# Kernel tuning notes

Hardware: AMD Instinct MI355X
Metric: run time of the kernel (lower is better)

## Reference

```python
import jax, jax.numpy as jnp
import numpy as np

N_NODES = 100_000
N_EDGES = 1_000_000
H = 128
NUM_STATES = 4
UPPER_T, LOWER_T, NUM_ITERS, TEMP_EVAL = 1.0, 0.1, 10000, 0.1


def temp_by_step(step, upper, lower, num_iters, temp_eval):
    # Python-level schedule: eval temp at step == -1, else linear anneal.
    if step == -1:
        return temp_eval
    frac = min(step / num_iters, 1.0)
    return upper + (lower - upper) * frac


def from_binary_states(states):
    # [*, k] bits -> integer id in [0, 2**k)
    weights = 2 ** jnp.arange(states.shape[-1])
    return (states * weights).sum(-1)


def setup_inputs() -> dict:
    key = jax.random.key(0)
    ks = jax.random.split(key, 20)
    N, E, h = N_NODES, N_EDGES, H
    node_states = jax.random.randint(ks[0], (N, NUM_STATES), 0, 2)
    edge_states = jax.random.randint(ks[1], (E, NUM_STATES), 0, 2)
    scalars = jax.random.normal(ks[2], (E, 1), jnp.float32)
    # first N edges are self-loops ordered by node id (required by the module's
    # node_scalars = scalars[src == dst] indexing convention)
    loops = jnp.arange(N)
    src = jax.random.randint(ks[3], (E - N,), 0, N)
    dst = jax.random.randint(ks[4], (E - N,), 0, N)
    dst = jnp.where(dst == src, (dst + 1) % N, dst)  # no accidental self-loops
    edge_index = jnp.stack([jnp.concatenate([loops, src]),
                            jnp.concatenate([loops, dst])])
    batched_reverse_idx = jax.random.randint(ks[5], (E,), 0, E)
    batch_scalars = jax.random.normal(ks[6], (E, 1, 1), jnp.float32)
    s = 0.02
    params = dict(
        node_emb=s * jax.random.normal(ks[7], (2 ** NUM_STATES, h), jnp.float32),
        edge_emb=s * jax.random.normal(ks[8], (2 ** NUM_STATES, h), jnp.float32),
        combine_W=s * jax.random.normal(ks[9], (2 * h, h), jnp.float32),
        combine_b=jnp.zeros((h,), jnp.float32),
        keep_W=s * jax.random.normal(ks[10], (h, 2), jnp.float32),
        keep_b=jnp.zeros((2,), jnp.float32),
        push_W=s * jax.random.normal(ks[11], (h, 2), jnp.float32),
        push_b=jnp.zeros((2,), jnp.float32),
        push_node_W=s * jax.random.normal(ks[12], (h, 2), jnp.float32),
        push_node_b=jnp.zeros((2,), jnp.float32),
        increment_W=s * jax.random.normal(ks[13], (h, 2), jnp.float32),
        increment_b=jnp.zeros((2,), jnp.float32),
    )
    return dict(node_states=node_states, edge_states=edge_states, scalars=scalars,
                edge_index=edge_index, batched_reverse_idx=batched_reverse_idx,
                batch_scalars=batch_scalars, processor_step=0, training_step=0,
                **params)


def reference(node_states, edge_states, scalars, edge_index, batched_reverse_idx,
              batch_scalars, processor_step, training_step,
              node_emb, edge_emb, combine_W, combine_b, keep_W, keep_b,
              push_W, push_b, push_node_W, push_node_b,
              increment_W, increment_b):
    N = node_states.shape[0]
    tau = temp_by_step(int(training_step), UPPER_T, LOWER_T, NUM_ITERS, TEMP_EVAL)
    # use_noise = config.use_noise (False) and training_step != -1 -> False

    node_fts = node_emb[from_binary_states(node_states)]   # [N, h]
    edge_fts = edge_emb[from_binary_states(edge_states)]   # [E, h]
    src, dst = edge_index[0], edge_index[1]
    fts = jnp.concatenate([edge_fts[batched_reverse_idx], node_fts[src]], axis=1)
    fts = fts @ combine_W + combine_b                       # [E, h]

    s = scalars.reshape(-1)                                 # [E]

    def pair_gumbel_first(W, b):
        # grouped (per-edge pair) softmax; take first component (== [::2])
        logits = (fts @ W + b) / tau                        # [E, 2]
        return jax.nn.softmax(logits, axis=-1)[:, 0]

    increment = 1.0 * pair_gumbel_first(increment_W, increment_b)
    keep = s * pair_gumbel_first(keep_W, keep_b)

    # push: first N edges are self-loops, self-loop of node i is edge i
    push_wo = pair_gumbel_first(push_W, push_b)
    push_w = pair_gumbel_first(push_node_W, push_node_b)
    node_scalars = s[:N]                                    # scalars at self-loops
    s_wo = s - node_scalars[dst]
    s_w = s_wo + node_scalars[src]
    acc = (jax.ops.segment_sum(push_wo * s_wo, dst, num_segments=N)
           + jax.ops.segment_sum(push_w * s_w, dst, num_segments=N))  # [N]
    edge_push = jnp.zeros_like(s).at[:N].set(acc)           # nonzero only on self-loops

    new_scalars = (increment + keep + edge_push)[:, None]   # [E, 1]
    target = batch_scalars[:, processor_step]               # [E, 1]
    loss = jnp.mean((target - new_scalars) ** 2)
    return new_scalars, loss
```

## Files before the change

kernel.cpp:

```cpp
#include <hip/hip_runtime.h>
#include <math.h>

#define N_NODES 100000
#define N_EDGES 1000000
#define HDIM 128
#define N_NONLOOP (N_EDGES - N_NODES)

typedef float  vfloat4 __attribute__((ext_vector_type(4)));

__device__ __forceinline__ float get_invtau(const int* __restrict__ training_step) {
    int step = training_step[0];
    float tau;
    if (step == -1) {
        tau = 0.1f;
    } else {
        float frac = fminf((float)step / 10000.0f, 1.0f);
        tau = 1.0f + (0.1f - 1.0f) * frac;
    }
    return 1.0f / tau;
}

__device__ __forceinline__ float wave_reduce(float v) {
    #pragma unroll
    for (int off = 32; off > 0; off >>= 1) v += __shfl_down(v, off, 64);
    return v;
}

__global__ __launch_bounds__(256) void precompute_tab1(
    const int* __restrict__ node_states,
    const float* __restrict__ s,
    const float* __restrict__ cW,
    const float* __restrict__ kW, const float* __restrict__ pW,
    const float* __restrict__ pnW, const float* __restrict__ iW,
    const int* __restrict__ tstep,
    float2* __restrict__ node_pack,
    float* __restrict__ acc,
    float* __restrict__ loss_out,
    float* __restrict__ uv)
{
    const int n = blockIdx.x * blockDim.x + threadIdx.x;
    if (n < N_NODES) {
        int4 st = ((const int4*)node_states)[n];
        const int idx = st.x + 2 * st.y + 4 * st.z + 8 * st.w;
        float2 np;
        np.x = s[n];
        np.y = __int_as_float(idx);
        node_pack[n] = np;
        acc[n] = 0.f;
    }
    if (n == 0) *loss_out = 0.f;

    if (blockIdx.x < 256) {
        __shared__ float wd[512];
        const float invtau = get_invtau(tstep);
        for (int i = threadIdx.x; i < 512; i += 256) {
            const int h = i >> 7, d = i & 127;
            const float* W = (h == 0) ? kW : (h == 1) ? pW : (h == 2) ? pnW : iW;
            wd[i] = W[2 * d] - W[2 * d + 1];
        }
        __syncthreads();

        const int row  = blockIdx.x * 4 + (threadIdx.x >> 6);
        const int lane = threadIdx.x & 63;
        const int half = row >> 9;
        const int r    = row & 511;
        const int h    = r >> 7, d = r & 127;
        const int cwrow = half * 128 + d;

        float p = cW[cwrow * 128 + lane]      * wd[h * 128 + lane]
                + cW[cwrow * 128 + 64 + lane] * wd[h * 128 + 64 + lane];
        p = wave_reduce(p);
        if (lane == 0) uv[row] = p * invtau;
    }
}

__global__ void tab_stage2(const float* __restrict__ node_emb,
                           const float* __restrict__ edge_emb,
                           const float* __restrict__ cb,
                           const float* __restrict__ kW, const float* __restrict__ kb,
                           const float* __restrict__ pW, const float* __restrict__ pb,
                           const float* __restrict__ pnW, const float* __restrict__ pnb,
                           const float* __restrict__ iW, const float* __restrict__ ib,
                           const int* __restrict__ tstep,
                           const float* __restrict__ uv,
                           float* __restrict__ tabs)
{
    const int w = blockIdx.x * 4 + (threadIdx.x >> 6);
    if (w >= 132) return;
    const int lane = threadIdx.x & 63;
    const float invtau = get_invtau(tstep);

    float p;
    if (w < 128) {
        const int isB = w >> 6, h = (w >> 4) & 3, i = w & 15;
        const float* emb = isB ? node_emb : edge_emb;
        const float* uvp = uv + isB * 512 + h * 128;
        p = emb[i * 128 + lane] * uvp[lane] + emb[i * 128 + 64 + lane] * uvp[64 + lane];
    } else {
        const int h = w - 128;
        const float* W = (h == 0) ? kW : (h == 1) ? pW : (h == 2) ? pnW : iW;
        p = cb[lane]      * (W[2 * lane] - W[2 * lane + 1])
          + cb[64 + lane] * (W[2 * (64 + lane)] - W[2 * (64 + lane) + 1]);
    }
    p = wave_reduce(p);
    if (lane == 0) {
        if (w < 64) {
            const int h = (w >> 4) & 3, i = w & 15;
            tabs[i * 4 + h] = p;
        } else if (w < 128) {
            const int h = (w >> 4) & 3, i = w & 15;
            tabs[64 + i * 4 + h] = p;
        } else {
            const int h = w - 128;
            const float* b = (h == 0) ? kb : (h == 1) ? pb : (h == 2) ? pnb : ib;
            tabs[128 + h] = (p + b[0] - b[1]) * invtau;
        }
    }
}

__global__ __launch_bounds__(256) void edge_kernel(
    const float* __restrict__ s,
    const int* __restrict__ src,
    const int* __restrict__ dst,
    const int* __restrict__ brev,
    const int* __restrict__ edge_states,
    const float2* __restrict__ node_pack,
    const float* __restrict__ tabs,
    const float* __restrict__ target,
    float* __restrict__ acc,
    float* __restrict__ out,
    float* __restrict__ loss_out)
{
    __shared__ float4 sf[33];
    if (threadIdx.x < 33) sf[threadIdx.x] = ((const float4*)tabs)[threadIdx.x];
    __syncthreads();

    const int t = blockIdx.x * blockDim.x + threadIdx.x;
    float lsum = 0.f;

    if (t < N_NONLOOP / 4) {
        const int g = (N_NODES / 4) + t;
        const int4   rv = ((const int4*)brev)[g];
        const int4   sr = ((const int4*)src)[g];
        const int4   ds = ((const int4*)dst)[g];
        const float4 sv = ((const float4*)s)[g];
        const vfloat4 tg = __builtin_nontemporal_load(&((const vfloat4*)target)[g]);

        const int rvv[4] = {rv.x, rv.y, rv.z, rv.w};
        const int srv[4] = {sr.x, sr.y, sr.z, sr.w};
        const int dsv[4] = {ds.x, ds.y, ds.z, ds.w};
        const float svv[4] = {sv.x, sv.y, sv.z, sv.w};
        const float tgv[4] = {tg.x, tg.y, tg.z, tg.w};

        int4  es[4];
        float2 np[4];
        float sd[4];
        #pragma unroll
        for (int j = 0; j < 4; ++j) {
            es[j] = ((const int4*)edge_states)[rvv[j]];
            np[j] = node_pack[srv[j]];
            sd[j] = node_pack[dsv[j]].x;
        }

        const float4 c4 = sf[32];
        float ov[4];
        #pragma unroll
        for (int j = 0; j < 4; ++j) {
            const int ei = es[j].x + 2 * es[j].y + 4 * es[j].z + 8 * es[j].w;
            const int   ni = __float_as_int(np[j].y);
            const float ss = np[j].x;
            const float4 a = sf[ei];
            const float4 b = sf[16 + ni];
            const float lk  = a.x + b.x + c4.x;
            const float lp  = a.y + b.y + c4.y;
            const float lpn = a.z + b.z + c4.z;
            const float li  = a.w + b.w + c4.w;
            const float pk  = 1.f / (1.f + __expf(-lk));
            const float pp  = 1.f / (1.f + __expf(-lp));
            const float ppn = 1.f / (1.f + __expf(-lpn));
            const float pi  = 1.f / (1.f + __expf(-li));

            const float s_wo = svv[j] - sd[j];
            const float s_w  = s_wo + ss;
            unsafeAtomicAdd(&acc[dsv[j]], pp * s_wo + ppn * s_w);

            ov[j] = pi + svv[j] * pk;
            const float d = tgv[j] - ov[j];
            lsum += d * d;
        }
        vfloat4 o4 = {ov[0], ov[1], ov[2], ov[3]};
        __builtin_nontemporal_store(o4, &((vfloat4*)out)[g]);
    }

    lsum = wave_reduce(lsum);
    __shared__ float wsum[4];
    const int lane = threadIdx.x & 63, wid = threadIdx.x >> 6;
    if (lane == 0) wsum[wid] = lsum;
    __syncthreads();
    if (threadIdx.x == 0) {
        const float tot = wsum[0] + wsum[1] + wsum[2] + wsum[3];
        atomicAdd(loss_out, tot * (1.0f / (float)N_EDGES));
    }
}

__global__ __launch_bounds__(256) void finalize_nodes(
    const int* __restrict__ brev,
    const int* __restrict__ edge_states,
    const float2* __restrict__ node_pack,
    const float* __restrict__ tabs,
    const float* __restrict__ target,
    const float* __restrict__ acc,
    float* __restrict__ out,
    float* __restrict__ loss_out)
{
    __shared__ float4 sf[33];
    if (threadIdx.x < 33) sf[threadIdx.x] = ((const float4*)tabs)[threadIdx.x];
    __syncthreads();

    const int n = blockIdx.x * blockDim.x + threadIdx.x;
    float sq = 0.f;
    if (n < N_NODES) {
        const int    rev = brev[n];
        const int4   est = ((const int4*)edge_states)[rev];
        const int    ei  = est.x + 2 * est.y + 4 * est.z + 8 * est.w;
        const float2 np  = node_pack[n];
        const int    ni  = __float_as_int(np.y);
        const float  sv  = np.x;

        const float4 a = sf[ei];
        const float4 b = sf[16 + ni];
        const float4 c4 = sf[32];
        const float lk  = a.x + b.x + c4.x;
        const float lpn = a.z + b.z + c4.z;
        const float li  = a.w + b.w + c4.w;
        const float pk  = 1.f / (1.f + __expf(-lk));
        const float ppn = 1.f / (1.f + __expf(-lpn));
        const float pi  = 1.f / (1.f + __expf(-li));

        const float v = pi + sv * (pk + ppn) + acc[n];
        out[n] = v;
        const float d = target[n] - v;
        sq = d * d;
    }
    sq = wave_reduce(sq);
    __shared__ float wsum[4];
    const int lane = threadIdx.x & 63, wid = threadIdx.x >> 6;
    if (lane == 0) wsum[wid] = sq;
    __syncthreads();
    if (threadIdx.x == 0) {
        const float tot = wsum[0] + wsum[1] + wsum[2] + wsum[3];
        atomicAdd(loss_out, tot * (1.0f / (float)N_EDGES));
    }
}

extern "C" void kernel_launch(void* const* d_in, const int* in_sizes, int n_in,
                              void* d_out, int out_size, void* d_ws, size_t ws_size,
                              hipStream_t stream) {
    const int*   node_states   = (const int*)d_in[0];
    const int*   edge_states   = (const int*)d_in[1];
    const float* scalars       = (const float*)d_in[2];
    const int*   edge_index    = (const int*)d_in[3];
    const int*   brev          = (const int*)d_in[4];
    const float* batch_scalars = (const float*)d_in[5];
    const int*   training_step = (const int*)d_in[7];
    const float* node_emb  = (const float*)d_in[8];
    const float* edge_emb  = (const float*)d_in[9];
    const float* combine_W = (const float*)d_in[10];
    const float* combine_b = (const float*)d_in[11];
    const float* keep_W  = (const float*)d_in[12];
    const float* keep_b  = (const float*)d_in[13];
    const float* push_W  = (const float*)d_in[14];
    const float* push_b  = (const float*)d_in[15];
    const float* pushn_W = (const float*)d_in[16];
    const float* pushn_b = (const float*)d_in[17];
    const float* inc_W   = (const float*)d_in[18];
    const float* inc_b   = (const float*)d_in[19];

    float* out = (float*)d_out;

    char* ws = (char*)d_ws;
    float*  tabs = (float*)ws;
    float*  uv   = (float*)(ws + 1024);
    float*  acc  = (float*)(ws + 1024 + 4096);
    float2* node_pack = (float2*)(ws + 1024 + 4096 + (size_t)N_NODES * 4);

    const int* srcp = edge_index;
    const int* dstp = edge_index + N_EDGES;

    precompute_tab1<<<(N_NODES + 255) / 256, 256, 0, stream>>>(
        node_states, scalars,
        combine_W, keep_W, push_W, pushn_W, inc_W, training_step,
        node_pack, acc, out + N_EDGES, uv);

    tab_stage2<<<33, 256, 0, stream>>>(node_emb, edge_emb, combine_b,
                                       keep_W, keep_b, push_W, push_b,
                                       pushn_W, pushn_b, inc_W, inc_b,
                                       training_step, uv, tabs);

    const int ethreads = N_NONLOOP / 4;
    edge_kernel<<<(ethreads + 255) / 256, 256, 0, stream>>>(
        scalars, srcp, dstp, brev, edge_states, node_pack, tabs, batch_scalars,
        acc, out, out + N_EDGES);

    finalize_nodes<<<(N_NODES + 255) / 256, 256, 0, stream>>>(
        brev, edge_states, node_pack, tabs, batch_scalars, acc, out, out + N_EDGES);
}
```

Measured before the change: 177.5 us.

## Privatize scatter-add accumulator per XCD with non-coherent local float atomics

Replaces the single device-wide node accumulator with eight copies, one per XCD chosen by reading the hardware XCC_ID register. Edge atomics now go to the XCD-local copy through a plain global_atomic_add_f32 without system scope, and the finalize kernel sums the eight partials. The aim is to keep atomics in each XCD's L2 instead of paying cross-die coherence costs. In exchange it zeroes and later reads eight times more accumulator memory, and correctness relies on the local L2 atomics becoming visible to the next kernel.

```diff
diff --git a/kernel.cpp b/kernel.cpp
--- a/kernel.cpp
+++ b/kernel.cpp
@@ -5,8 +5,19 @@
 #define N_EDGES 1000000
 #define HDIM 128
 #define N_NONLOOP (N_EDGES - N_NODES)
-
-typedef float  vfloat4 __attribute__((ext_vector_type(4)));
+#define N_XCD 8
+
+typedef float vfloat4 __attribute__((ext_vector_type(4)));
+
+__device__ __forceinline__ int xcc_id() {
+    unsigned v;
+    asm volatile("s_getreg_b32 %0, hwreg(HW_REG_XCC_ID)" : "=s"(v));
+    return (int)(v & (N_XCD - 1));
+}
+
+__device__ __forceinline__ void xcd_local_fadd(float* p, float v) {
+    asm volatile("global_atomic_add_f32 %0, %1, off" : : "v"(p), "v"(v) : "memory");
+}
 
 __device__ __forceinline__ float get_invtau(const int* __restrict__ training_step) {
     int step = training_step[0];
@@ -34,11 +45,12 @@
     const float* __restrict__ pnW, const float* __restrict__ iW,
     const int* __restrict__ tstep,
     float2* __restrict__ node_pack,
-    float* __restrict__ acc,
+    float* __restrict__ acc8,
     float* __restrict__ loss_out,
     float* __restrict__ uv)
 {
     const int n = blockIdx.x * blockDim.x + threadIdx.x;
+    const int NT = gridDim.x * blockDim.x;
     if (n < N_NODES) {
         int4 st = ((const int4*)node_states)[n];
         const int idx = st.x + 2 * st.y + 4 * st.z + 8 * st.w;
@@ -46,8 +58,8 @@
         np.x = s[n];
         np.y = __int_as_float(idx);
         node_pack[n] = np;
-        acc[n] = 0.f;
-    }
+    }
+    for (int i = n; i < N_XCD * N_NODES; i += NT) acc8[i] = 0.f;
     if (n == 0) *loss_out = 0.f;
 
     if (blockIdx.x < 256) {
@@ -127,13 +139,15 @@
     const float2* __restrict__ node_pack,
     const float* __restrict__ tabs,
     const float* __restrict__ target,
-    float* __restrict__ acc,
+    float* __restrict__ acc8,
     float* __restrict__ out,
     float* __restrict__ loss_out)
 {
     __shared__ float4 sf[33];
     if (threadIdx.x < 33) sf[threadIdx.x] = ((const float4*)tabs)[threadIdx.x];
     __syncthreads();
+
+    float* myacc = acc8 + (size_t)xcc_id() * N_NODES;
 
     const int t = blockIdx.x * blockDim.x + threadIdx.x;
     float lsum = 0.f;
@@ -152,9 +166,9 @@
         const float svv[4] = {sv.x, sv.y, sv.z, sv.w};
         const float tgv[4] = {tg.x, tg.y, tg.z, tg.w};
 
-        int4  es[4];
+        int4   es[4];
         float2 np[4];
-        float sd[4];
+        float  sd[4];
         #pragma unroll
         for (int j = 0; j < 4; ++j) {
             es[j] = ((const int4*)edge_states)[rvv[j]];
@@ -182,7 +196,7 @@
 
             const float s_wo = svv[j] - sd[j];
             const float s_w  = s_wo + ss;
-            unsafeAtomicAdd(&acc[dsv[j]], pp * s_wo + ppn * s_w);
+            xcd_local_fadd(&myacc[dsv[j]], pp * s_wo + ppn * s_w);
 
             ov[j] = pi + svv[j] * pk;
             const float d = tgv[j] - ov[j];
@@ -191,6 +205,8 @@
         vfloat4 o4 = {ov[0], ov[1], ov[2], ov[3]};
         __builtin_nontemporal_store(o4, &((vfloat4*)out)[g]);
     }
+
+    asm volatile("s_waitcnt vmcnt(0)" ::: "memory");
 
     lsum = wave_reduce(lsum);
     __shared__ float wsum[4];
@@ -209,7 +225,7 @@
     const float2* __restrict__ node_pack,
     const float* __restrict__ tabs,
     const float* __restrict__ target,
-    const float* __restrict__ acc,
+    const float* __restrict__ acc8,
     float* __restrict__ out,
     float* __restrict__ loss_out)
 {
@@ -227,6 +243,10 @@
         const int    ni  = __float_as_int(np.y);
         const float  sv  = np.x;
 
+        float accv = 0.f;
+        #pragma unroll
+        for (int x = 0; x < N_XCD; ++x) accv += acc8[(size_t)x * N_NODES + n];
+
         const float4 a = sf[ei];
         const float4 b = sf[16 + ni];
         const float4 c4 = sf[32];
@@ -237,7 +257,7 @@
         const float ppn = 1.f / (1.f + __expf(-lpn));
         const float pi  = 1.f / (1.f + __expf(-li));
 
-        const float v = pi + sv * (pk + ppn) + acc[n];
+        const float v = pi + sv * (pk + ppn) + accv;
         out[n] = v;
         const float d = target[n] - v;
         sq = d * d;
@@ -281,8 +301,8 @@
     char* ws = (char*)d_ws;
     float*  tabs = (float*)ws;
     float*  uv   = (float*)(ws + 1024);
-    float*  acc  = (float*)(ws + 1024 + 4096);
-    float2* node_pack = (float2*)(ws + 1024 + 4096 + (size_t)N_NODES * 4);
+    float2* node_pack = (float2*)(ws + 1024 + 4096);
+    float*  acc8 = (float*)(ws + 1024 + 4096 + (size_t)N_NODES * 8);
 
     const int* srcp = edge_index;
     const int* dstp = edge_index + N_EDGES;
@@ -290,7 +310,7 @@
     precompute_tab1<<<(N_NODES + 255) / 256, 256, 0, stream>>>(
         node_states, scalars,
         combine_W, keep_W, push_W, pushn_W, inc_W, training_step,
-        node_pack, acc, out + N_EDGES, uv);
+        node_pack, acc8, out + N_EDGES, uv);
 
     tab_stage2<<<33, 256, 0, stream>>>(node_emb, edge_emb, combine_b,
                                        keep_W, keep_b, push_W, push_b,
@@ -300,8 +320,8 @@
     const int ethreads = N_NONLOOP / 4;
     edge_kernel<<<(ethreads + 255) / 256, 256, 0, stream>>>(
         scalars, srcp, dstp, brev, edge_states, node_pack, tabs, batch_scalars,
-        acc, out, out + N_EDGES);
+        acc8, out, out + N_EDGES);
 
     finalize_nodes<<<(N_NODES + 255) / 256, 256, 0, stream>>>(
-        brev, edge_states, node_pack, tabs, batch_scalars, acc, out, out + N_EDGES);
-}
+        brev, edge_states, node_pack, tabs, batch_scalars, acc8, out, out + N_EDGES);
+}
```

After: 180.6 us. Within noise of the previous version (+1.7%).
